# Kernel optimization log

Hardware: AMD Instinct MI355X
Metric: run time of the kernel (lower is better)

The kernel has to match this reference:

```python
import jax, jax.numpy as jnp
import numpy as np

N = 524288
B, F, H, W = 2, 4, 64, 512
S = B * F * H * W  # dense voxel segment space
EPS = 1e-5


def _bn(x, g, b):
    # BatchNorm1d in training mode: normalize over the point dim with biased var
    m = x.mean(0)
    v = jnp.mean((x - m) ** 2, 0)
    return (x - m) / jnp.sqrt(v + EPS) * g + b


def setup_inputs() -> dict:
    key = jax.random.key(0)
    ks = jax.random.split(key, 20)
    pts = jax.random.normal(ks[0], (N, 4), dtype=jnp.float32) * 10.0
    bcol = jax.random.randint(ks[1], (N, 1), 0, B)
    fcol = jax.random.randint(ks[2], (N, 1), 0, F)
    hcol = jax.random.randint(ks[3], (N, 1), 0, H)
    wcol = jax.random.randint(ks[4], (N, 1), 0, W)
    coors = jnp.concatenate([bcol, fcol, hcol, wcol], -1).astype(jnp.int32)
    # original reads batch_size/frame_size from coors[-1]
    coors = coors.at[-1].set(jnp.array([B - 1, F - 1, H - 1, W - 1], dtype=jnp.int32))
    s = 0.02
    p = {
        'pre_gamma': jnp.ones((8,), jnp.float32),
        'pre_beta': jnp.zeros((8,), jnp.float32),
        'W1': jax.random.normal(ks[5], (8, 64), jnp.float32) * s,
        'g1': jnp.ones((64,), jnp.float32), 'b1': jnp.zeros((64,), jnp.float32),
        'W2': jax.random.normal(ks[6], (64, 128), jnp.float32) * s,
        'g2': jnp.ones((128,), jnp.float32), 'b2': jnp.zeros((128,), jnp.float32),
        'W3': jax.random.normal(ks[7], (128, 256), jnp.float32) * s,
        'g3': jnp.ones((256,), jnp.float32), 'b3': jnp.zeros((256,), jnp.float32),
        'W4': jax.random.normal(ks[8], (256, 256), jnp.float32) * s,
        'b4': jnp.zeros((256,), jnp.float32),
        'Wc': jax.random.normal(ks[9], (256, 64), jnp.float32) * s,
        'bc': jnp.zeros((64,), jnp.float32),
    }
    return {'pts': pts, 'pts_coors': coors, **p}


def reference(pts, pts_coors, pre_gamma, pre_beta, W1, g1, b1, W2, g2, b2,
              W3, g3, b3, W4, b4, Wc, bc):
    c = pts_coors
    lin = ((c[:, 0] * F + c[:, 1]) * H + c[:, 2]) * W + c[:, 3]  # (N,)
    counts = jax.ops.segment_sum(jnp.ones((pts.shape[0],), pts.dtype), lin, num_segments=S)
    # with_distance
    dist = jnp.linalg.norm(pts[:, :3], axis=1, keepdims=True)
    # with_cluster_center: scatter_mean then gather
    vsum = jax.ops.segment_sum(pts, lin, num_segments=S)
    vmean = vsum / jnp.clip(counts, 1.0)[:, None]
    f_cluster = pts[:, :3] - vmean[lin][:, :3]
    feats = jnp.concatenate([pts, dist, f_cluster], -1)  # (N, 8)
    feats = _bn(feats, pre_gamma, pre_beta)  # pre_norm
    x = jax.nn.relu(_bn(feats @ W1, g1, b1))
    x = jax.nn.relu(_bn(x @ W2, g2, b2))
    x = jax.nn.relu(_bn(x @ W3, g3, b3))
    point_feats = x @ W4 + b4  # (N, 256)
    # scatter_max over voxels
    seg = jax.ops.segment_max(point_feats, lin, num_segments=S)
    mask = (counts > 0)[:, None]
    voxel_feats = jnp.where(mask, seg, 0.0)
    comp = jax.nn.relu(voxel_feats @ Wc + bc)
    comp = jnp.where(mask, comp, 0.0)  # empty voxels stay zero in stack_frame
    stack = comp.reshape(B, F, H, W, -1)  # (B, F, H, W, Cc)
    residual = jnp.concatenate([stack[:, -1] - stack[:, f] for f in range(F - 1)], -1)
    residual_img = jnp.transpose(residual, (0, 3, 1, 2))  # (B, C, H, W)
    return residual_img
```

## Files before the change

### kernel.cpp

```cpp
#include <hip/hip_runtime.h>
#include <hip/hip_bf16.h>
#include <stdint.h>

typedef unsigned int u32;
typedef unsigned short u16;
typedef __attribute__((ext_vector_type(8))) short bf16x8;
typedef __attribute__((ext_vector_type(4))) float f32x4;

#define NPTS 524288
#define FF 4
#define HH 64
#define WW 512
#define SS 262144
#define EPSV 1e-5f
#define NB 8192
#define RCAP 80
#define VCAP 80

__device__ __forceinline__ float bf2f(u16 h){ return __uint_as_float(((u32)h)<<16); }
__device__ __forceinline__ u16 f2bf(float f){
  u32 u = __float_as_uint(f);
  return (u16)((u + 0x7FFFu + ((u>>16)&1u)) >> 16);
}

__device__ __forceinline__ void point_feats(int p, const float* __restrict__ pts,
    const u32* __restrict__ lin, const u32* __restrict__ counts,
    const float* __restrict__ vsum, float f[8], u32* vout){
  float4 pt = ((const float4*)pts)[p];
  u32 v = lin[p];
  float cnt = fmaxf((float)counts[v], 1.0f);
  float inv = 1.0f/cnt;
  float mx = vsum[v*3+0]*inv, my = vsum[v*3+1]*inv, mz = vsum[v*3+2]*inv;
  float dist = sqrtf(pt.x*pt.x + pt.y*pt.y + pt.z*pt.z);
  f[0]=pt.x; f[1]=pt.y; f[2]=pt.z; f[3]=pt.w; f[4]=dist;
  f[5]=pt.x-mx; f[6]=pt.y-my; f[7]=pt.z-mz;
  *vout = v;
}

__global__ __launch_bounds__(256) void k_lin(const float* __restrict__ pts,
                                             const int* __restrict__ coors,
                                             u32* __restrict__ lin,
                                             u32* __restrict__ counts,
                                             float* __restrict__ vsum){
  int p = blockIdx.x*256 + threadIdx.x;
  int4 c = ((const int4*)coors)[p];
  u32 v = ((u32)((c.x*FF + c.y)*HH + c.z))*WW + (u32)c.w;
  lin[p] = v;
  atomicAdd(&counts[v], 1u);
  float4 pt = ((const float4*)pts)[p];
  atomicAdd(&vsum[v*3+0], pt.x);
  atomicAdd(&vsum[v*3+1], pt.y);
  atomicAdd(&vsum[v*3+2], pt.z);
}

__global__ __launch_bounds__(256) void k_scan_a(const u32* __restrict__ counts,
                                                u32* __restrict__ blockSums){
  __shared__ u32 lds[256];
  int b = blockIdx.x, t = threadIdx.x;
  uint4 c4 = ((const uint4*)counts)[b*256 + t];
  lds[t] = c4.x + c4.y + c4.z + c4.w;
  __syncthreads();
  for(int s=128; s>0; s>>=1){ if(t<s) lds[t] += lds[t+s]; __syncthreads(); }
  if(t==0) blockSums[b] = lds[0];
}

__global__ void k_scan_b(u32* blockSums){
  if(threadIdx.x==0){
    u32 run = 0;
    for(int i=0;i<256;i++){ u32 v = blockSums[i]; blockSums[i] = run; run += v; }
  }
}

__global__ __launch_bounds__(256) void k_scan_c(const u32* __restrict__ counts,
                                                const u32* __restrict__ blockSums,
                                                u32* __restrict__ offsets,
                                                u32* __restrict__ cursor){
  __shared__ u32 lds[256];
  int b = blockIdx.x, t = threadIdx.x;
  uint4 c4 = ((const uint4*)counts)[b*256 + t];
  u32 mysum = c4.x + c4.y + c4.z + c4.w;
  lds[t] = mysum;
  __syncthreads();
  for(int d=1; d<256; d<<=1){
    u32 v = (t>=d) ? lds[t-d] : 0u;
    __syncthreads();
    lds[t] += v;
    __syncthreads();
  }
  u32 off = blockSums[b] + (t>0 ? lds[t-1] : 0u);
  u32 base = (u32)(b*1024 + t*4);
  offsets[base+0]=off; cursor[base+0]=off; off += c4.x;
  offsets[base+1]=off; cursor[base+1]=off; off += c4.y;
  offsets[base+2]=off; cursor[base+2]=off; off += c4.z;
  offsets[base+3]=off; cursor[base+3]=off; off += c4.w;
  if(base+4 == SS) offsets[SS] = off;
}

__global__ __launch_bounds__(256) void k_scatter(const u32* __restrict__ lin,
                                                 u32* __restrict__ cursor,
                                                 u32* __restrict__ order){
  int p = blockIdx.x*256 + threadIdx.x;
  u32 v = lin[p];
  u32 pos = atomicAdd(&cursor[v], 1u);
  order[pos] = p;
}

__global__ __launch_bounds__(256) void k_prep(const float* __restrict__ W2,
    const float* __restrict__ W3, const float* __restrict__ W4,
    const float* __restrict__ Wc,
    u16* __restrict__ W2t, u16* __restrict__ W3t, u16* __restrict__ W4t,
    u16* __restrict__ Wct){
  int i = blockIdx.x*256 + threadIdx.x;
  if(i < 8192){
    int k = i >> 7, n = i & 127;
    W2t[n*64 + k] = f2bf(W2[i]);
  } else if(i < 8192+32768){
    int j = i - 8192;
    int k = j >> 8, n = j & 255;
    W3t[n*128 + k] = f2bf(W3[j]);
  } else if(i < 8192+32768+65536){
    int j = i - (8192+32768);
    int k = j >> 8, n = j & 255;
    W4t[n*256 + k] = f2bf(W4[j]);
  } else if(i < 8192+32768+65536+16384){
    int j = i - (8192+32768+65536);
    int k = j >> 6, n = j & 63;
    Wct[n*256 + k] = f2bf(Wc[j]);
  }
}

__global__ __launch_bounds__(256) void k_stats0(const float* __restrict__ pts,
    const u32* __restrict__ lin, const u32* __restrict__ counts,
    const float* __restrict__ vsum, float* __restrict__ sum0, float* __restrict__ sq0){
  int p = blockIdx.x*256 + threadIdx.x;
  float f[8]; u32 v;
  point_feats(p, pts, lin, counts, vsum, f, &v);
  __shared__ float lsum[4][8], lsq[4][8];
  int lane = threadIdx.x & 63, wv = threadIdx.x >> 6;
  #pragma unroll
  for(int c=0;c<8;c++){
    float s = f[c], q = f[c]*f[c];
    #pragma unroll
    for(int d=32; d; d>>=1){ s += __shfl_xor(s,d); q += __shfl_xor(q,d); }
    if(lane==0){ lsum[wv][c]=s; lsq[wv][c]=q; }
  }
  __syncthreads();
  if(threadIdx.x<8){
    float s=0.f,q=0.f;
    for(int g=0;g<4;g++){ s+=lsum[g][threadIdx.x]; q+=lsq[g][threadIdx.x]; }
    atomicAdd(&sum0[threadIdx.x], s);
    atomicAdd(&sq0[threadIdx.x], q);
  }
}

__global__ void k_fold(const float* __restrict__ sum, const float* __restrict__ sq,
                       const float* __restrict__ g, const float* __restrict__ b,
                       float* __restrict__ a, float* __restrict__ c, int C){
  int i = blockIdx.x*64 + threadIdx.x;
  if(i < C){
    float m = sum[i]*(1.0f/NPTS);
    float v = sq[i]*(1.0f/NPTS) - m*m;
    v = fmaxf(v, 0.0f);
    float ai = g[i] / sqrtf(v + EPSV);
    a[i] = ai;
    c[i] = b[i] - m*ai;
  }
}

__global__ __launch_bounds__(256) void k_stats1(const float* __restrict__ pts,
    const u32* __restrict__ lin, const u32* __restrict__ counts,
    const float* __restrict__ vsum,
    const float* __restrict__ a0, const float* __restrict__ c0,
    const float* __restrict__ W1, float* __restrict__ sum1, float* __restrict__ sq1){
  __shared__ float ws[4][64], wq[4][64];
  int t = threadIdx.x;
  int p = blockIdx.x*256 + t;
  float f[8]; u32 v;
  point_feats(p, pts, lin, counts, vsum, f, &v);
  float y0[8];
  #pragma unroll
  for(int k=0;k<8;k++) y0[k] = a0[k]*f[k] + c0[k];
  float z[64];
  #pragma unroll
  for(int j=0;j<64;j++){
    float s=0.f;
    #pragma unroll
    for(int k=0;k<8;k++) s += y0[k]*W1[k*64+j];
    z[j]=s;
  }
  int lane = t&63, wv = t>>6;
  float ks=0.f, kq=0.f;
  #pragma unroll
  for(int c=0;c<64;c++){
    float s=z[c], q=z[c]*z[c];
    #pragma unroll
    for(int d=1; d<64; d<<=1){ s+=__shfl_xor(s,d); q+=__shfl_xor(q,d); }
    if(lane==c){ ks=s; kq=q; }
  }
  ws[wv][lane]=ks; wq[wv][lane]=kq;
  __syncthreads();
  if(t<64){
    float S=ws[0][t]+ws[1][t]+ws[2][t]+ws[3][t];
    float Q=wq[0][t]+wq[1][t]+wq[2][t]+wq[3][t];
    atomicAdd(&sum1[t],S); atomicAdd(&sq1[t],Q);
  }
}

__global__ __launch_bounds__(256,2) void k_mstats2(
    const float* __restrict__ pts, const u32* __restrict__ lin,
    const u32* __restrict__ counts, const float* __restrict__ vsum,
    const float* __restrict__ a0, const float* __restrict__ c0,
    const float* __restrict__ a1, const float* __restrict__ c1,
    const float* __restrict__ W1, const u16* __restrict__ W2t,
    float* __restrict__ sum2, float* __restrict__ sq2){
  __shared__ u16 T1[256*72];
  int tid = threadIdx.x, lane = tid&63, wid = tid>>6, l15 = lane&15, lg = lane>>4;
  float s2[2] = {0.f,0.f}, q2[2] = {0.f,0.f};

  for(int cch=0; cch<4; cch++){
    int p = blockIdx.x*1024 + cch*256 + tid;
    float f[8]; u32 v;
    point_feats(p, pts, lin, counts, vsum, f, &v);
    float y0[8];
    #pragma unroll
    for(int k=0;k<8;k++) y0[k] = a0[k]*f[k] + c0[k];
    u32 pk[32];
    #pragma unroll
    for(int jj=0;jj<32;jj++){
      float s0=0.f, s1=0.f;
      #pragma unroll
      for(int k=0;k<8;k++){ s0 += y0[k]*W1[k*64+2*jj]; s1 += y0[k]*W1[k*64+2*jj+1]; }
      float v0f = fmaxf(a1[2*jj]*s0   + c1[2*jj],   0.f);
      float v1f = fmaxf(a1[2*jj+1]*s1 + c1[2*jj+1], 0.f);
      pk[jj] = (u32)f2bf(v0f) | ((u32)f2bf(v1f)<<16);
    }
    __syncthreads();
    {
      uint4* dst = (uint4*)&T1[tid*72];
      #pragma unroll
      for(int q=0;q<8;q++) dst[q] = make_uint4(pk[4*q],pk[4*q+1],pk[4*q+2],pk[4*q+3]);
    }
    __syncthreads();
    #pragma unroll
    for(int ci=0; ci<2; ci++){
      int ch = (wid + 4*ci)*16 + l15;
      const u16* wb = W2t + (size_t)ch*64 + lg*8;
      bf16x8 b0 = *(const bf16x8*)(wb);
      bf16x8 b1 = *(const bf16x8*)(wb + 32);
      for(int rt=0; rt<16; rt++){
        const u16* ap = T1 + (rt*16 + l15)*72 + lg*8;
        bf16x8 af0 = *(const bf16x8*)(ap);
        bf16x8 af1 = *(const bf16x8*)(ap + 32);
        f32x4 acc = {0.f,0.f,0.f,0.f};
        acc = __builtin_amdgcn_mfma_f32_16x16x32_bf16(af0, b0, acc, 0,0,0);
        acc = __builtin_amdgcn_mfma_f32_16x16x32_bf16(af1, b1, acc, 0,0,0);
        #pragma unroll
        for(int i=0;i<4;i++){ s2[ci] += acc[i]; q2[ci] += acc[i]*acc[i]; }
      }
    }
  }
  #pragma unroll
  for(int ci=0; ci<2; ci++){
    float s = s2[ci], q = q2[ci];
    s += __shfl_xor(s,16); s += __shfl_xor(s,32);
    q += __shfl_xor(q,16); q += __shfl_xor(q,32);
    if(lg == 0){
      int ch = (wid + 4*ci)*16 + l15;
      atomicAdd(&sum2[ch], s);
      atomicAdd(&sq2[ch], q);
    }
  }
}

__global__ __launch_bounds__(256,1) void k_chain2(
    const float* __restrict__ pts, const u32* __restrict__ lin,
    const u32* __restrict__ counts, const float* __restrict__ vsum,
    const u32* __restrict__ order,
    const float* __restrict__ a0, const float* __restrict__ c0,
    const float* __restrict__ a1, const float* __restrict__ c1,
    const float* __restrict__ a2, const float* __restrict__ c2,
    const float* __restrict__ W1, const u16* __restrict__ W2t,
    const u16* __restrict__ W3t,
    u32* __restrict__ y2s,
    float* __restrict__ sum3, float* __restrict__ sq3){
  __shared__ u16 T1[256*72];
  __shared__ u16 T2[256*136];
  int tid = threadIdx.x, lane = tid&63, wid = tid>>6, l15 = lane&15, lg = lane>>4;
  float s3[4] = {0.f,0.f,0.f,0.f}, q3[4] = {0.f,0.f,0.f,0.f};

  for(int cch=0; cch<4; cch++){
    int rr = blockIdx.x*1024 + cch*256 + tid;
    int p = (int)order[rr];
    float f[8]; u32 v;
    point_feats(p, pts, lin, counts, vsum, f, &v);
    float y0[8];
    #pragma unroll
    for(int k=0;k<8;k++) y0[k] = a0[k]*f[k] + c0[k];
    u32 pk[32];
    #pragma unroll
    for(int jj=0;jj<32;jj++){
      float s0=0.f, s1=0.f;
      #pragma unroll
      for(int k=0;k<8;k++){ s0 += y0[k]*W1[k*64+2*jj]; s1 += y0[k]*W1[k*64+2*jj+1]; }
      float v0f = fmaxf(a1[2*jj]*s0   + c1[2*jj],   0.f);
      float v1f = fmaxf(a1[2*jj+1]*s1 + c1[2*jj+1], 0.f);
      pk[jj] = (u32)f2bf(v0f) | ((u32)f2bf(v1f)<<16);
    }
    __syncthreads();
    {
      uint4* dst = (uint4*)&T1[tid*72];
      #pragma unroll
      for(int q=0;q<8;q++) dst[q] = make_uint4(pk[4*q],pk[4*q+1],pk[4*q+2],pk[4*q+3]);
    }
    __syncthreads();
    #pragma unroll
    for(int ci=0; ci<2; ci++){
      int ch = (wid + 4*ci)*16 + l15;
      const u16* wb = W2t + (size_t)ch*64 + lg*8;
      bf16x8 b0 = *(const bf16x8*)(wb);
      bf16x8 b1 = *(const bf16x8*)(wb + 32);
      float a2v = a2[ch], c2v = c2[ch];
      for(int rt=0; rt<16; rt++){
        const u16* ap = T1 + (rt*16 + l15)*72 + lg*8;
        bf16x8 af0 = *(const bf16x8*)(ap);
        bf16x8 af1 = *(const bf16x8*)(ap + 32);
        f32x4 acc = {0.f,0.f,0.f,0.f};
        acc = __builtin_amdgcn_mfma_f32_16x16x32_bf16(af0, b0, acc, 0,0,0);
        acc = __builtin_amdgcn_mfma_f32_16x16x32_bf16(af1, b1, acc, 0,0,0);
        int rbase = rt*16 + lg*4;
        #pragma unroll
        for(int i=0;i<4;i++)
          T2[(rbase+i)*136 + ch] = f2bf(fmaxf(a2v*acc[i] + c2v, 0.f));
      }
    }
    __syncthreads();
    {
      const u32* T2w = (const u32*)T2;
      u32 base = (u32)blockIdx.x*1024u + (u32)cch*256u;
      for(int i=tid; i<256*64; i+=256){
        int row = i>>6, w = i&63;
        y2s[(size_t)(base+row)*64 + w] = T2w[row*68 + w];
      }
    }
    #pragma unroll
    for(int ci=0; ci<4; ci++){
      int ch = (wid + 4*ci)*16 + l15;
      const u16* wb = W3t + (size_t)ch*128 + lg*8;
      bf16x8 b[4];
      #pragma unroll
      for(int ks=0; ks<4; ks++) b[ks] = *(const bf16x8*)(wb + ks*32);
      for(int rt=0; rt<16; rt++){
        const u16* ap = T2 + (rt*16 + l15)*136 + lg*8;
        f32x4 acc = {0.f,0.f,0.f,0.f};
        #pragma unroll
        for(int ks=0; ks<4; ks++){
          bf16x8 af = *(const bf16x8*)(ap + ks*32);
          acc = __builtin_amdgcn_mfma_f32_16x16x32_bf16(af, b[ks], acc, 0,0,0);
        }
        #pragma unroll
        for(int i=0;i<4;i++){ s3[ci] += acc[i]; q3[ci] += acc[i]*acc[i]; }
      }
    }
  }
  #pragma unroll
  for(int ci=0; ci<4; ci++){
    float s = s3[ci], q = q3[ci];
    s += __shfl_xor(s,16); s += __shfl_xor(s,32);
    q += __shfl_xor(q,16); q += __shfl_xor(q,32);
    if(lg == 0){
      int ch = (wid + 4*ci)*16 + l15;
      atomicAdd(&sum3[ch], s);
      atomicAdd(&sq3[ch], q);
    }
  }
}

__global__ __launch_bounds__(256,2) void k_mega4(
    const u32* __restrict__ offsets, const u32* __restrict__ y2s,
    const float* __restrict__ a3, const float* __restrict__ c3,
    const u16* __restrict__ W3t, const u16* __restrict__ W4t,
    const u16* __restrict__ Wct,
    const float* __restrict__ b4, const float* __restrict__ bc,
    u16* __restrict__ comp){
  __shared__ __align__(16) char SM[65664];
  u16* T3  = (u16*)(SM);
  u16* T2s = (u16*)(SM + 42240);
  u16* Tz  = (u16*)(SM + 42240);
  u16* TA  = (u16*)(SM + 53760);
  u32* vst = (u32*)(SM + 65280);
  u32* hdr = (u32*)(SM + 65616);

  int tid = threadIdx.x, lane = tid & 63, wid = tid >> 6;
  int l15 = lane & 15, lg = lane >> 4;

  if(tid == 0){
    u32 t0 = (u32)blockIdx.x * 64u;
    u32 lo=0, hi=SS;
    while(lo<hi){ u32 mid=(lo+hi)>>1; if(offsets[mid] < t0) lo=mid+1; else hi=mid; }
    u32 vlo = lo, vhi;
    if(blockIdx.x == NB-1) vhi = SS;
    else {
      u32 t1 = t0 + 64u;
      lo = vlo; hi = SS;
      while(lo<hi){ u32 mid=(lo+hi)>>1; if(offsets[mid] < t1) lo=mid+1; else hi=mid; }
      vhi = lo;
    }
    hdr[0]=vlo; hdr[1]=vhi; hdr[2]=offsets[vlo]; hdr[3]=offsets[vhi];
  }
  __syncthreads();
  u32 vlo=hdr[0], vhi=hdr[1], start=hdr[2], end=hdr[3];
  int R = (int)(end - start); if(R > RCAP) R = RCAP;
  int V = (int)(vhi - vlo);   if(V > VCAP) V = VCAP;

  if(tid <= VCAP){
    u32 o = (tid <= V) ? offsets[vlo + tid] : end;
    int s = (int)(o - start); if(s > RCAP) s = RCAP;
    vst[tid] = (u32)s;
  }

  {
    u32* T2w = (u32*)T2s;
    for(int i=tid; i<RCAP*64; i+=256){
      int row = i>>6, w = i&63;
      u32 val = (row < R) ? y2s[(size_t)(start+row)*64 + w] : 0u;
      T2w[row*68 + w] = val;
    }
  }
  __syncthreads();

  for(int ci=0; ci<4; ci++){
    int ch = (wid + 4*ci)*16 + l15;
    const u16* wb = W3t + (size_t)ch*128 + lg*8;
    bf16x8 b[4];
    #pragma unroll
    for(int ks=0; ks<4; ks++) b[ks] = *(const bf16x8*)(wb + ks*32);
    float a3v = a3[ch], c3v = c3[ch];
    for(int rt=0; rt<5; rt++){
      const u16* ap = T2s + (rt*16 + l15)*136 + lg*8;
      f32x4 acc = {0.f,0.f,0.f,0.f};
      #pragma unroll
      for(int ks=0; ks<4; ks++){
        bf16x8 af = *(const bf16x8*)(ap + ks*32);
        acc = __builtin_amdgcn_mfma_f32_16x16x32_bf16(af, b[ks], acc, 0,0,0);
      }
      int rbase = rt*16 + lg*4;
      #pragma unroll
      for(int i=0;i<4;i++)
        T3[(rbase+i)*264 + ch] = f2bf(fmaxf(a3v*acc[i] + c3v, 0.f));
    }
  }
  __syncthreads();

  f32x4 acc5[5];
  #pragma unroll
  for(int i=0;i<5;i++) acc5[i] = (f32x4){0.f,0.f,0.f,0.f};
  int ch4 = wid*16 + l15;

  for(int oc=0; oc<4; oc++){
    {
      int chg = oc*64 + ch4;
      const u16* wb = W4t + (size_t)chg*256 + lg*8;
      bf16x8 b[8];
      #pragma unroll
      for(int ks=0; ks<8; ks++) b[ks] = *(const bf16x8*)(wb + ks*32);
      for(int rt=0; rt<5; rt++){
        const u16* ap = T3 + (rt*16 + l15)*264 + lg*8;
        f32x4 acc = {0.f,0.f,0.f,0.f};
        #pragma unroll
        for(int ks=0; ks<8; ks++){
          bf16x8 af = *(const bf16x8*)(ap + ks*32);
          acc = __builtin_amdgcn_mfma_f32_16x16x32_bf16(af, b[ks], acc, 0,0,0);
        }
        int rbase = rt*16 + lg*4;
        #pragma unroll
        for(int i=0;i<4;i++)
          Tz[(rbase+i)*72 + ch4] = f2bf(acc[i]);
      }
    }
    __syncthreads();
    for(int i=tid; i<VCAP*64; i+=256){
      int v = i>>6, k = i&63;
      u32 r0 = vst[v], r1 = vst[v+1];
      u16 outv = 0;
      if(r1 > r0){
        float m = -3.0e38f;
        for(u32 r=r0; r<r1; r++) m = fmaxf(m, bf2f(Tz[r*72+k]));
        outv = f2bf(m + b4[oc*64+k]);
      }
      TA[v*72+k] = outv;
    }
    __syncthreads();
    {
      const u16* wb = Wct + (size_t)ch4*256 + oc*64 + lg*8;
      bf16x8 b0 = *(const bf16x8*)(wb);
      bf16x8 b1 = *(const bf16x8*)(wb + 32);
      #pragma unroll
      for(int vt=0; vt<5; vt++){
        const u16* ap = TA + (vt*16 + l15)*72 + lg*8;
        bf16x8 af0 = *(const bf16x8*)(ap);
        bf16x8 af1 = *(const bf16x8*)(ap + 32);
        acc5[vt] = __builtin_amdgcn_mfma_f32_16x16x32_bf16(af0, b0, acc5[vt], 0,0,0);
        acc5[vt] = __builtin_amdgcn_mfma_f32_16x16x32_bf16(af1, b1, acc5[vt], 0,0,0);
      }
    }
    __syncthreads();
  }

  {
    float bcv = bc[ch4];
    #pragma unroll
    for(int vt=0; vt<5; vt++){
      int vbase = vt*16 + lg*4;
      #pragma unroll
      for(int i=0;i<4;i++){
        int vox = vbase + i;
        if(vox < V){
          bool nz = vst[vox+1] > vst[vox];
          float val = nz ? fmaxf(acc5[vt][i] + bcv, 0.f) : 0.f;
          comp[(size_t)(vlo+vox)*64 + ch4] = f2bf(val);
        }
      }
    }
  }
}

__global__ __launch_bounds__(256) void k_resid(const u16* __restrict__ comp,
                                               float* __restrict__ out){
  __shared__ u32 cl[4*128*32];
  int t = threadIdx.x;
  int blk = blockIdx.x;
  int wq = blk & 3, h = (blk>>2) & 63, b = blk>>8;
  int w0 = wq*128;
  for(int fr=0; fr<4; fr++){
    const u32* src = (const u32*)comp + ((size_t)(((b*4+fr)*64 + h)*512 + w0))*32;
    for(int i=t; i<4096; i+=256){
      int vox = i>>5, wd = i&31;
      cl[fr*4096 + vox*32 + (wd ^ (vox&31))] = src[i];
    }
  }
  __syncthreads();
  int wl = t & 127, half = t >> 7;
  int mv = wl & 31;
  for(int ch = half; ch < 64; ch += 2){
    u32 wr3 = cl[3*4096 + wl*32 + ((ch>>1) ^ mv)];
    float r3 = bf2f((ch&1) ? (u16)(wr3>>16) : (u16)(wr3&0xFFFFu));
    #pragma unroll
    for(int fr=0; fr<3; fr++){
      u32 wrf = cl[fr*4096 + wl*32 + ((ch>>1) ^ mv)];
      float vf = bf2f((ch&1) ? (u16)(wrf>>16) : (u16)(wrf&0xFFFFu));
      out[(((size_t)(b*192 + fr*64 + ch))*64 + h)*512 + w0 + wl] = r3 - vf;
    }
  }
}

extern "C" void kernel_launch(void* const* d_in, const int* in_sizes, int n_in,
                              void* d_out, int out_size, void* d_ws, size_t ws_size,
                              hipStream_t stream){
  const float* pts  = (const float*)d_in[0];
  const int*  coors = (const int*)d_in[1];
  const float* g0 = (const float*)d_in[2];
  const float* b0 = (const float*)d_in[3];
  const float* W1 = (const float*)d_in[4];
  const float* g1 = (const float*)d_in[5];
  const float* b1 = (const float*)d_in[6];
  const float* W2 = (const float*)d_in[7];
  const float* g2 = (const float*)d_in[8];
  const float* b2 = (const float*)d_in[9];
  const float* W3 = (const float*)d_in[10];
  const float* g3 = (const float*)d_in[11];
  const float* b3 = (const float*)d_in[12];
  const float* W4 = (const float*)d_in[13];
  const float* b4 = (const float*)d_in[14];
  const float* Wc = (const float*)d_in[15];
  const float* bc = (const float*)d_in[16];
  float* out = (float*)d_out;
  (void)in_sizes; (void)n_in; (void)out_size; (void)ws_size;

  char* ws = (char*)d_ws;
  size_t off = 0;
  auto alloc = [&](size_t bytes)->void*{
    void* p = ws + off;
    off += (bytes + 255) & ~(size_t)255;
    return p;
  };
  u32*  counts  = (u32*)alloc((size_t)SS*4);
  float* vsum   = (float*)alloc((size_t)SS*3*4);
  float* stats  = (float*)alloc(8192);
  size_t zero_bytes = off;
  u32*  lin     = (u32*)alloc((size_t)NPTS*4);
  u32*  offsets = (u32*)alloc((size_t)(SS+1)*4);
  u32*  cursor  = (u32*)alloc((size_t)SS*4);
  u32*  order   = (u32*)alloc((size_t)NPTS*4);
  u32*  blockSums = (u32*)alloc(1024);
  u16*  comp    = (u16*)alloc((size_t)SS*64*2);
  u16*  W2t = (u16*)alloc(8192*2);
  u16*  W3t = (u16*)alloc(32768*2);
  u16*  W4t = (u16*)alloc(65536*2);
  u16*  Wct = (u16*)alloc(16384*2);
  u32*  y2s = (u32*)alloc((size_t)NPTS*64*4);

  float* sum0=stats+0,   *sq0=stats+8,    *a0=stats+16,   *c0=stats+24;
  float* sum1=stats+32,  *sq1=stats+96,   *a1=stats+160,  *c1=stats+224;
  float* sum2=stats+288, *sq2=stats+416,  *a2=stats+544,  *c2=stats+672;
  float* sum3=stats+800, *sq3=stats+1056, *a3=stats+1312, *c3=stats+1568;

  hipMemsetAsync(d_ws, 0, zero_bytes, stream);

  k_prep   <<<480, 256,0,stream>>>(W2, W3, W4, Wc, W2t, W3t, W4t, Wct);
  k_lin    <<<2048,256,0,stream>>>(pts, coors, lin, counts, vsum);
  k_scan_a <<<256, 256,0,stream>>>(counts, blockSums);
  k_scan_b <<<1,   64, 0,stream>>>(blockSums);
  k_scan_c <<<256, 256,0,stream>>>(counts, blockSums, offsets, cursor);
  k_scatter<<<2048,256,0,stream>>>(lin, cursor, order);

  k_stats0 <<<2048,256,0,stream>>>(pts, lin, counts, vsum, sum0, sq0);
  k_fold   <<<1,   64, 0,stream>>>(sum0, sq0, g0, b0, a0, c0, 8);
  k_stats1 <<<2048,256,0,stream>>>(pts, lin, counts, vsum, a0, c0, W1, sum1, sq1);
  k_fold   <<<1,   64, 0,stream>>>(sum1, sq1, g1, b1, a1, c1, 64);
  k_mstats2<<<512, 256,0,stream>>>(pts, lin, counts, vsum, a0,c0,a1,c1, W1, W2t, sum2, sq2);
  k_fold   <<<2,   64, 0,stream>>>(sum2, sq2, g2, b2, a2, c2, 128);
  k_chain2 <<<512, 256,0,stream>>>(pts, lin, counts, vsum, order,
                                   a0,c0,a1,c1,a2,c2, W1, W2t, W3t,
                                   y2s, sum3, sq3);
  k_fold   <<<4,   64, 0,stream>>>(sum3, sq3, g3, b3, a3, c3, 256);

  k_mega4  <<<NB,  256,0,stream>>>(offsets, y2s, a3,c3, W3t, W4t, Wct, b4, bc, comp);
  k_resid  <<<512, 256,0,stream>>>(comp, out);
}
```

Measured before the change: 1.191 ms.

## Split fused voxel MLP kernel into dense point GEMM and segment-max stages

Replaces the fused per-voxel kernel with two kernels. The first runs layers 3 and 4 as dense tiled MFMA GEMMs over all points and writes a channel-major bf16 z4 buffer. The second does the per-voxel segment max over that buffer, then the compression GEMM. This removes the irregular per-voxel work inside the GEMM stage, but adds a 256 MB intermediate write and read. The split path only runs if the workspace is large enough, otherwise it falls back to the old kernel.

```diff
diff --git a/kernel.cpp b/kernel.cpp
--- a/kernel.cpp
+++ b/kernel.cpp
@@ -375,6 +375,119 @@
   }
 }
 
+__global__ __launch_bounds__(512,4) void k_z4(
+    const u32* __restrict__ y2s,
+    const float* __restrict__ a3, const float* __restrict__ c3,
+    const u16* __restrict__ W3t, const u16* __restrict__ W4t,
+    u16* __restrict__ z4t){
+  __shared__ u16 T3[128*264];
+  int tid = threadIdx.x, lane = tid & 63, wid = tid >> 6;
+  int l15 = lane & 15, lg = lane >> 4;
+  size_t row0 = (size_t)blockIdx.x * 128;
+
+  for(int ci=0; ci<2; ci++){
+    int ch = (wid + 8*ci)*16 + l15;
+    const u16* wb = W3t + (size_t)ch*128 + lg*8;
+    bf16x8 b[4];
+    #pragma unroll
+    for(int ks=0; ks<4; ks++) b[ks] = *(const bf16x8*)(wb + ks*32);
+    float a3v = a3[ch], c3v = c3[ch];
+    for(int rt=0; rt<8; rt++){
+      const u16* ap = (const u16*)y2s + (row0 + rt*16 + l15)*128 + lg*8;
+      f32x4 acc = {0.f,0.f,0.f,0.f};
+      #pragma unroll
+      for(int ks=0; ks<4; ks++){
+        bf16x8 af = *(const bf16x8*)(ap + ks*32);
+        acc = __builtin_amdgcn_mfma_f32_16x16x32_bf16(af, b[ks], acc, 0,0,0);
+      }
+      int rbase = rt*16 + lg*4;
+      #pragma unroll
+      for(int i=0;i<4;i++)
+        T3[(rbase+i)*264 + ch] = f2bf(fmaxf(a3v*acc[i] + c3v, 0.f));
+    }
+  }
+  __syncthreads();
+
+  for(int ci=0; ci<2; ci++){
+    int ch = (wid + 8*ci)*16 + l15;
+    const u16* wb = W4t + (size_t)ch*256 + lg*8;
+    bf16x8 b[8];
+    #pragma unroll
+    for(int ks=0; ks<8; ks++) b[ks] = *(const bf16x8*)(wb + ks*32);
+    for(int rt=0; rt<8; rt++){
+      const u16* ap = T3 + (rt*16 + l15)*264 + lg*8;
+      f32x4 acc = {0.f,0.f,0.f,0.f};
+      #pragma unroll
+      for(int ks=0; ks<8; ks++){
+        bf16x8 af = *(const bf16x8*)(ap + ks*32);
+        acc = __builtin_amdgcn_mfma_f32_16x16x32_bf16(af, b[ks], acc, 0,0,0);
+      }
+      size_t r = row0 + (size_t)rt*16 + lg*4;
+      u32 p0 = (u32)f2bf(acc[0]) | ((u32)f2bf(acc[1])<<16);
+      u32 p1 = (u32)f2bf(acc[2]) | ((u32)f2bf(acc[3])<<16);
+      u32* dst = (u32*)(z4t + (size_t)ch*NPTS + r);
+      dst[0] = p0; dst[1] = p1;
+    }
+  }
+}
+
+__global__ __launch_bounds__(256,4) void k_segcomp(
+    const u32* __restrict__ offsets, const u16* __restrict__ z4t,
+    const float* __restrict__ b4, const u16* __restrict__ Wct,
+    const float* __restrict__ bc, u16* __restrict__ comp){
+  __shared__ u16 TA[64*264];
+  __shared__ u32 voff[65];
+  __shared__ float bb[256];
+  int tid = threadIdx.x, lane = tid & 63, wid = tid >> 6;
+  int l15 = lane & 15, lg = lane >> 4;
+  u32 v0 = (u32)blockIdx.x * 64u;
+
+  if(tid < 65) voff[tid] = offsets[v0 + tid];
+  bb[tid] = b4[tid];
+  __syncthreads();
+
+  {
+    int k = tid;
+    const u16* col = z4t + (size_t)k*NPTS;
+    for(int v=0; v<64; v++){
+      u32 r0 = voff[v], r1 = voff[v+1];
+      u16 o = 0;
+      if(r1 > r0){
+        float m = -3.0e38f;
+        for(u32 r=r0; r<r1; r++) m = fmaxf(m, bf2f(col[r]));
+        o = f2bf(m + bb[k]);
+      }
+      TA[v*264 + k] = o;
+    }
+  }
+  __syncthreads();
+
+  int ch4 = wid*16 + l15;
+  const u16* wb = Wct + (size_t)ch4*256 + lg*8;
+  bf16x8 b[8];
+  #pragma unroll
+  for(int ks=0; ks<8; ks++) b[ks] = *(const bf16x8*)(wb + ks*32);
+  float bcv = bc[ch4];
+  #pragma unroll
+  for(int vt=0; vt<4; vt++){
+    const u16* ap = TA + (vt*16 + l15)*264 + lg*8;
+    f32x4 acc = {0.f,0.f,0.f,0.f};
+    #pragma unroll
+    for(int ks=0; ks<8; ks++){
+      bf16x8 af = *(const bf16x8*)(ap + ks*32);
+      acc = __builtin_amdgcn_mfma_f32_16x16x32_bf16(af, b[ks], acc, 0,0,0);
+    }
+    int vbase = vt*16 + lg*4;
+    #pragma unroll
+    for(int i=0;i<4;i++){
+      int vox = vbase + i;
+      bool nz = voff[vox+1] > voff[vox];
+      float val = nz ? fmaxf(acc[i] + bcv, 0.f) : 0.f;
+      comp[(size_t)(v0+vox)*64 + ch4] = f2bf(val);
+    }
+  }
+}
+
 __global__ __launch_bounds__(256,2) void k_mega4(
     const u32* __restrict__ offsets, const u32* __restrict__ y2s,
     const float* __restrict__ a3, const float* __restrict__ c3,
@@ -574,7 +687,7 @@
   const float* Wc = (const float*)d_in[15];
   const float* bc = (const float*)d_in[16];
   float* out = (float*)d_out;
-  (void)in_sizes; (void)n_in; (void)out_size; (void)ws_size;
+  (void)in_sizes; (void)n_in; (void)out_size;
 
   char* ws = (char*)d_ws;
   size_t off = 0;
@@ -598,6 +711,8 @@
   u16*  W4t = (u16*)alloc(65536*2);
   u16*  Wct = (u16*)alloc(16384*2);
   u32*  y2s = (u32*)alloc((size_t)NPTS*64*4);
+  u16*  z4t = (u16*)alloc((size_t)NPTS*256*2);
+  bool use_split = (off <= ws_size);
 
   float* sum0=stats+0,   *sq0=stats+8,    *a0=stats+16,   *c0=stats+24;
   float* sum1=stats+32,  *sq1=stats+96,   *a1=stats+160,  *c1=stats+224;
@@ -624,6 +739,11 @@
                                    y2s, sum3, sq3);
   k_fold   <<<4,   64, 0,stream>>>(sum3, sq3, g3, b3, a3, c3, 256);
 
-  k_mega4  <<<NB,  256,0,stream>>>(offsets, y2s, a3,c3, W3t, W4t, Wct, b4, bc, comp);
+  if(use_split){
+    k_z4     <<<4096,512,0,stream>>>(y2s, a3, c3, W3t, W4t, z4t);
+    k_segcomp<<<4096,256,0,stream>>>(offsets, z4t, b4, Wct, bc, comp);
+  } else {
+    k_mega4  <<<NB,  256,0,stream>>>(offsets, y2s, a3,c3, W3t, W4t, Wct, b4, bc, comp);
+  }
   k_resid  <<<512, 256,0,stream>>>(comp, out);
 }
```

Result: no change. 1.191 ms (+0.0%).

## Use 512-thread blocks in fused voxel kernel, splitting row tiles across wave halves

Applied to the files above, without the earlier changes.

The fused W3/W4/maxpool/compress kernel now runs 8 waves per block instead of 4. Waves 0-3 and 4-7 each cover half of the row and voxel tiles in the W4 and compress GEMMs, and the W3 GEMM spreads its channel groups over all 8 waves. The trailing barrier in the output-channel loop is removed, since the next Tz write does not overlap the TA buffer being read. The aim is to put twice as many waves per CU under the same LDS footprint and hide more latency. The (512,4) launch bound caps the register budget and could force spills, and the 3+2 tile split leaves the two wave halves with unequal work.

```diff
diff --git a/kernel.cpp b/kernel.cpp
--- a/kernel.cpp
+++ b/kernel.cpp
@@ -375,7 +375,7 @@
   }
 }
 
-__global__ __launch_bounds__(256,2) void k_mega4(
+__global__ __launch_bounds__(512,4) void k_mega5(
     const u32* __restrict__ offsets, const u32* __restrict__ y2s,
     const float* __restrict__ a3, const float* __restrict__ c3,
     const u16* __restrict__ W3t, const u16* __restrict__ W4t,
@@ -392,6 +392,8 @@
 
   int tid = threadIdx.x, lane = tid & 63, wid = tid >> 6;
   int l15 = lane & 15, lg = lane >> 4;
+  int cg = wid & 3, rh = wid >> 2;
+  int nvt = rh ? 2 : 3, vt0 = rh ? 3 : 0;
 
   if(tid == 0){
     u32 t0 = (u32)blockIdx.x * 64u;
@@ -420,7 +422,7 @@
 
   {
     u32* T2w = (u32*)T2s;
-    for(int i=tid; i<RCAP*64; i+=256){
+    for(int i=tid; i<RCAP*64; i+=512){
       int row = i>>6, w = i&63;
       u32 val = (row < R) ? y2s[(size_t)(start+row)*64 + w] : 0u;
       T2w[row*68 + w] = val;
@@ -428,8 +430,8 @@
   }
   __syncthreads();
 
-  for(int ci=0; ci<4; ci++){
-    int ch = (wid + 4*ci)*16 + l15;
+  for(int ci=0; ci<2; ci++){
+    int ch = (wid + 8*ci)*16 + l15;
     const u16* wb = W3t + (size_t)ch*128 + lg*8;
     bf16x8 b[4];
     #pragma unroll
@@ -451,10 +453,10 @@
   }
   __syncthreads();
 
-  f32x4 acc5[5];
+  f32x4 acc3[3];
   #pragma unroll
-  for(int i=0;i<5;i++) acc5[i] = (f32x4){0.f,0.f,0.f,0.f};
-  int ch4 = wid*16 + l15;
+  for(int i=0;i<3;i++) acc3[i] = (f32x4){0.f,0.f,0.f,0.f};
+  int ch4 = cg*16 + l15;
 
   for(int oc=0; oc<4; oc++){
     {
@@ -463,7 +465,8 @@
       bf16x8 b[8];
       #pragma unroll
       for(int ks=0; ks<8; ks++) b[ks] = *(const bf16x8*)(wb + ks*32);
-      for(int rt=0; rt<5; rt++){
+      int rtB = rh ? 3 : 0, rtE = rh ? 5 : 3;
+      for(int rt=rtB; rt<rtE; rt++){
         const u16* ap = T3 + (rt*16 + l15)*264 + lg*8;
         f32x4 acc = {0.f,0.f,0.f,0.f};
         #pragma unroll
@@ -478,7 +481,7 @@
       }
     }
     __syncthreads();
-    for(int i=tid; i<VCAP*64; i+=256){
+    for(int i=tid; i<VCAP*64; i+=512){
       int v = i>>6, k = i&63;
       u32 r0 = vst[v], r1 = vst[v+1];
       u16 outv = 0;
@@ -495,29 +498,34 @@
       bf16x8 b0 = *(const bf16x8*)(wb);
       bf16x8 b1 = *(const bf16x8*)(wb + 32);
       #pragma unroll
-      for(int vt=0; vt<5; vt++){
-        const u16* ap = TA + (vt*16 + l15)*72 + lg*8;
-        bf16x8 af0 = *(const bf16x8*)(ap);
-        bf16x8 af1 = *(const bf16x8*)(ap + 32);
-        acc5[vt] = __builtin_amdgcn_mfma_f32_16x16x32_bf16(af0, b0, acc5[vt], 0,0,0);
-        acc5[vt] = __builtin_amdgcn_mfma_f32_16x16x32_bf16(af1, b1, acc5[vt], 0,0,0);
-      }
-    }
-    __syncthreads();
+      for(int s=0; s<3; s++){
+        if(s < nvt){
+          int vt = vt0 + s;
+          const u16* ap = TA + (vt*16 + l15)*72 + lg*8;
+          bf16x8 af0 = *(const bf16x8*)(ap);
+          bf16x8 af1 = *(const bf16x8*)(ap + 32);
+          acc3[s] = __builtin_amdgcn_mfma_f32_16x16x32_bf16(af0, b0, acc3[s], 0,0,0);
+          acc3[s] = __builtin_amdgcn_mfma_f32_16x16x32_bf16(af1, b1, acc3[s], 0,0,0);
+        }
+      }
+    }
   }
 
   {
     float bcv = bc[ch4];
     #pragma unroll
-    for(int vt=0; vt<5; vt++){
-      int vbase = vt*16 + lg*4;
-      #pragma unroll
-      for(int i=0;i<4;i++){
-        int vox = vbase + i;
-        if(vox < V){
-          bool nz = vst[vox+1] > vst[vox];
-          float val = nz ? fmaxf(acc5[vt][i] + bcv, 0.f) : 0.f;
-          comp[(size_t)(vlo+vox)*64 + ch4] = f2bf(val);
+    for(int s=0; s<3; s++){
+      if(s < nvt){
+        int vt = vt0 + s;
+        int vbase = vt*16 + lg*4;
+        #pragma unroll
+        for(int i=0;i<4;i++){
+          int vox = vbase + i;
+          if(vox < V){
+            bool nz = vst[vox+1] > vst[vox];
+            float val = nz ? fmaxf(acc3[s][i] + bcv, 0.f) : 0.f;
+            comp[(size_t)(vlo+vox)*64 + ch4] = f2bf(val);
+          }
         }
       }
     }
@@ -624,6 +632,6 @@
                                    y2s, sum3, sq3);
   k_fold   <<<4,   64, 0,stream>>>(sum3, sq3, g3, b3, a3, c3, 256);
 
-  k_mega4  <<<NB,  256,0,stream>>>(offsets, y2s, a3,c3, W3t, W4t, Wct, b4, bc, comp);
+  k_mega5  <<<NB,  512,0,stream>>>(offsets, y2s, a3,c3, W3t, W4t, Wct, b4, bc, comp);
   k_resid  <<<512, 256,0,stream>>>(comp, out);
 }
```

New measurement: 1.106 ms. 7.1% less time.
